# Kernel optimization log

Hardware: AMD Instinct MI355X
Metric: run time of the kernel (lower is better)

The kernel has to match this reference:

```python
import jax, jax.numpy as jnp
import numpy as np

B, T, N, H, L, K, E, KSEL = 16, 24, 2000, 64, 2, 2, 3, 2
OUT_LEN = 24
NUM_MAT = 1 + 2 * K  # identity + K powers of each of the 2 supports


def _rw(adj):
    # random-walk matrix D^{-1} A
    d = adj.sum(axis=1)
    return adj / jnp.where(d == 0, 1.0, d)[:, None]


def _dconv(xh, A_q, A_h, W, b):
    # k-hop dual-direction diffusion convolution; xh: [b,n,f]
    feats = [xh]
    for A in (A_q, A_h):
        cur = xh
        for _ in range(K):
            cur = jnp.einsum('nm,bmf->bnf', A, cur)
            feats.append(cur)
    return jnp.concatenate(feats, axis=-1) @ W + b


def _cell(x, h, A_q, A_h, Wg, bg, Wc, bc):
    # DCRNN (diffusion-conv GRU) cell
    xh = jnp.concatenate([x, h], axis=-1)
    ru = jax.nn.sigmoid(_dconv(xh, A_q, A_h, Wg, bg))
    r, u = jnp.split(ru, 2, axis=-1)
    c = jnp.tanh(_dconv(jnp.concatenate([x, r * h], axis=-1), A_q, A_h, Wc, bc))
    return u * h + (1.0 - u) * c


def setup_inputs() -> dict:
    key = jax.random.key(0)
    ks = jax.random.split(key, 24)
    s = 0.02
    nrm = lambda k, shp: (jax.random.normal(k, shp) * s).astype(jnp.float32)
    adj = (jax.random.uniform(ks[0], (N, N)) * (jax.random.uniform(ks[1], (N, N)) < 0.05)).astype(jnp.float32)
    x_enc = jax.random.normal(ks[2], (B, T, N, 1), dtype=jnp.float32)
    x_enc = x_enc * (jax.random.uniform(ks[3], (B, T, N, 1)) < 0.7)
    x_dec = jax.random.normal(ks[4], (B, OUT_LEN, N, 1), dtype=jnp.float32)

    def cell_p(k, fin):
        k1, k2 = jax.random.split(k)
        fcat = NUM_MAT * (fin + H)
        return (nrm(k1, (fcat, 2 * H)), jnp.zeros(2 * H, jnp.float32),
                nrm(k2, (fcat, H)), jnp.zeros(H, jnp.float32))

    e0 = cell_p(ks[5], 1)
    e1 = cell_p(ks[6], H)
    d0 = cell_p(ks[7], 1)
    d1 = cell_p(ks[8], H)
    return dict(
        adj=adj, x_enc=x_enc, x_dec=x_dec,
        gate_w1=nrm(ks[9], (T, H)), gate_b1=jnp.zeros(H, jnp.float32),
        gate_w2=nrm(ks[10], (H, E)), gate_b2=jnp.zeros(E, jnp.float32),
        ew_mean=nrm(ks[11], (T, T)), eb_mean=jnp.zeros(T, jnp.float32),
        ew_wmean=nrm(ks[12], (T, T)), eb_wmean=jnp.zeros(T, jnp.float32),
        ew_diff=nrm(ks[13], (T, T)), eb_diff=jnp.zeros(T, jnp.float32),
        enc0_Wg=e0[0], enc0_bg=e0[1], enc0_Wc=e0[2], enc0_bc=e0[3],
        enc1_Wg=e1[0], enc1_bg=e1[1], enc1_Wc=e1[2], enc1_bc=e1[3],
        dec0_Wg=d0[0], dec0_bg=d0[1], dec0_Wc=d0[2], dec0_bc=d0[3],
        dec1_Wg=d1[0], dec1_bg=d1[1], dec1_Wc=d1[2], dec1_bc=d1[3],
        fc_w=nrm(ks[14], (H, 1)), fc_b=jnp.zeros(1, jnp.float32),
        epoch=10,
    )


def reference(adj, x_enc, x_dec, gate_w1, gate_b1, gate_w2, gate_b2,
              ew_mean, eb_mean, ew_wmean, eb_wmean, ew_diff, eb_diff,
              enc0_Wg, enc0_bg, enc0_Wc, enc0_bc, enc1_Wg, enc1_bg, enc1_Wc, enc1_bc,
              dec0_Wg, dec0_bg, dec0_Wc, dec0_bc, dec1_Wg, dec1_bg, dec1_Wc, dec1_bc,
              fc_w, fc_b, epoch):
    A_q = _rw(adj)
    A_h = _rw(adj.T)

    # ---- DataPreparation: MoE-gated graph imputation ----
    x = jnp.transpose(x_enc[..., 0], (0, 2, 1))  # [b, n, t]
    g = jax.nn.relu(x @ gate_w1 + gate_b1)
    logits = g @ gate_w2 + gate_b2               # [b, n, E]
    top, idx = jax.lax.top_k(logits, KSEL)
    w = jax.nn.softmax(top, axis=-1)
    gate = (w[..., None] * jax.nn.one_hot(idx, E, dtype=x.dtype)).sum(axis=-2)  # [b,n,E]

    adj_ns = adj * (1.0 - jnp.eye(N, dtype=adj.dtype))
    deg_bin = (adj_ns > 0).astype(x.dtype)
    A_mean = deg_bin / jnp.maximum(deg_bin.sum(axis=1, keepdims=True), 1.0)
    rs = adj_ns.sum(axis=1, keepdims=True)
    A_wmean = adj_ns / jnp.where(rs == 0, 1.0, rs)
    A_diff = _rw(adj_ns)

    outs = [jnp.einsum('nm,bmt->bnt', A_agg, x) @ W + b
            for A_agg, W, b in ((A_mean, ew_mean, eb_mean),
                                (A_wmean, ew_wmean, eb_wmean),
                                (A_diff, ew_diff, eb_diff))]
    combined = (gate[..., None] * jnp.stack(outs, axis=2)).sum(axis=2)  # [b,n,t]
    x = jnp.where(x == 0, combined, x)
    x_imp = jnp.transpose(x, (0, 2, 1))[..., None]  # [b,t,n,1]

    # ---- Encoder: scan over time, 2 DCRNN layers ----
    enc_params = ((enc0_Wg, enc0_bg, enc0_Wc, enc0_bc),
                  (enc1_Wg, enc1_bg, enc1_Wc, enc1_bc))

    def enc_step(h, xt):
        inp = xt
        hs = []
        for l in range(L):
            nh = _cell(inp, h[l], A_q, A_h, *enc_params[l])
            inp = nh
            hs.append(nh)
        return jnp.stack(hs), None

    h0 = jnp.zeros((L, B, N, H), x_imp.dtype)
    hT, _ = jax.lax.scan(enc_step, h0, jnp.transpose(x_imp, (1, 0, 2, 3)))

    dec_params = ((dec0_Wg, dec0_bg, dec0_Wc, dec0_bc),
                  (dec1_Wg, dec1_bg, dec1_Wc, dec1_bc))

    def dec_step(carry, _):
        inp, h = carry
        hs = []
        for l in range(L):
            nh = _cell(inp, h[l], A_q, A_h, *dec_params[l])
            inp = nh
            hs.append(nh)
        out = nh @ fc_w + fc_b  # [b,n,1]
        return (out, jnp.stack(hs)), out

    _, outs_t = jax.lax.scan(dec_step, (x_imp[:, -1], hT), None, length=OUT_LEN)
    return jnp.transpose(outs_t, (1, 0, 2, 3))  # [b, out_len, n, 1]
```

## Files before the change

kernel.cpp:

```cpp
#include <hip/hip_runtime.h>

#define NROW 2000
#define NB   16
#define NT   24
#define NH   64
#define NM   (NROW*NB)
#define HOPLDS (NROW*64)
#define ENT_CAP 262144

typedef _Float16 h16;
typedef __attribute__((ext_vector_type(2))) _Float16 h16x2;
typedef __attribute__((ext_vector_type(8))) _Float16 h16x8;
typedef __attribute__((ext_vector_type(4))) float    f32x4;

__device__ __forceinline__ h16x2 bc_h2(unsigned int u){ union{unsigned int u; h16x2 h;} c; c.u=u; return c.h; }

__global__ __launch_bounds__(256) void k_count(const float* adj, int* cnt_q, int* cnt_h, int* cnt_ns,
    float* rsum_q, float* rsum_h, float* rsum_ns, int* deg_ns){
  int wid = (blockIdx.x*256 + threadIdx.x)>>6;
  int lane = threadIdx.x & 63;
  int kind = wid / NROW, n = wid - kind*NROW;
  int cnt = 0; float sum = 0.f;
  for (int c = lane; c < NROW; c += 64){
    float v = (kind==1) ? adj[(size_t)c*NROW + n] : adj[(size_t)n*NROW + c];
    if (kind==2 && c==n) v = 0.f;
    cnt += (v != 0.f); sum += v;
  }
  for (int off=32; off; off>>=1){ cnt += __shfl_down(cnt,off); sum += __shfl_down(sum,off); }
  if (lane==0){
    int pc = (cnt+7)&~7;
    if (kind==0){ cnt_q[n]=pc; rsum_q[n]=sum; }
    else if (kind==1){ cnt_h[n]=pc; rsum_h[n]=sum; }
    else { cnt_ns[n]=pc; rsum_ns[n]=sum; deg_ns[n]=cnt; }
  }
}

__global__ __launch_bounds__(1024) void k_scan(const int* cq, const int* ch, const int* cn,
    int* rq, int* rh, int* rn){
  __shared__ int s0[2048], s1[2048], s2[2048];
  int t = threadIdx.x;
  for (int a=0;a<2;a++){ int i=t+a*1024; s0[i]= i<NROW?cq[i]:0; s1[i]= i<NROW?ch[i]:0; s2[i]= i<NROW?cn[i]:0; }
  __syncthreads();
  for (int off=1; off<2048; off<<=1){
    int v0[2],v1[2],v2[2];
    for (int a=0;a<2;a++){ int i=t+a*1024; v0[a]= i>=off? s0[i-off]:0; v1[a]= i>=off? s1[i-off]:0; v2[a]= i>=off? s2[i-off]:0; }
    __syncthreads();
    for (int a=0;a<2;a++){ int i=t+a*1024; s0[i]+=v0[a]; s1[i]+=v1[a]; s2[i]+=v2[a]; }
    __syncthreads();
  }
  for (int a=0;a<2;a++){ int i=t+a*1024; if (i<=NROW){ rq[i]= i? s0[i-1]:0; rh[i]= i? s1[i-1]:0; rn[i]= i? s2[i-1]:0; } }
}

__device__ __forceinline__ uint2 mk_ent(int c, float a){
  h16 h = (h16)a;
  unsigned short us = __builtin_bit_cast(unsigned short, h);
  return make_uint2((unsigned int)(c*64), (unsigned int)us * 0x10001u);
}

__global__ __launch_bounds__(256) void k_fill(const float* adj, const int* rptr_q, const int* rptr_h, const int* rptr_ns,
    const float* rsum_q, const float* rsum_h, const float* rsum_ns, const int* deg_ns,
    uint2* ent_q, uint2* ent_h, uint2* ent_m, uint2* ent_w){
  int wid = (blockIdx.x*256 + threadIdx.x)>>6;
  int lane = threadIdx.x & 63;
  int kind = wid / NROW, n = wid - kind*NROW;
  const int* rp = (kind==0)?rptr_q:(kind==1)?rptr_h:rptr_ns;
  int p = rp[n], pend = rp[n+1];
  float inv, invm = 0.f;
  if (kind==0){ float d = rsum_q[n]; inv = d!=0.f?1.f/d:0.f; }
  else if (kind==1){ float d = rsum_h[n]; inv = d!=0.f?1.f/d:0.f; }
  else { float d = rsum_ns[n]; inv = d!=0.f?1.f/d:0.f; int dg = deg_ns[n]; invm = 1.f/(float)(dg>1?dg:1); }
  int base = 0;
  unsigned long long below = (1ull<<lane)-1ull;
  for (int c0=0; c0<NROW; c0+=64){
    int c = c0+lane; float v = 0.f;
    if (c < NROW){ v = (kind==1)? adj[(size_t)c*NROW+n] : adj[(size_t)n*NROW+c]; if (kind==2 && c==n) v = 0.f; }
    unsigned long long m = __ballot(v != 0.f);
    if (v != 0.f){
      int pos = p + base + __popcll(m & below);
      if (kind==2){ ent_w[pos] = mk_ent(c, v*inv); ent_m[pos] = mk_ent(c, invm); }
      else if (kind==0) ent_q[pos] = mk_ent(c, v*inv);
      else              ent_h[pos] = mk_ent(c, v*inv);
    }
    base += __popcll(m);
  }
  for (int i = p+base+lane; i < pend; i += 64){
    uint2 z = make_uint2(0u,0u);
    if (kind==2){ ent_w[i]=z; ent_m[i]=z; } else if (kind==0) ent_q[i]=z; else ent_h[i]=z;
  }
}

struct HopJob { const h16* X; const int* rptr; const uint2* ent; h16* out; };

__device__ __forceinline__ void proc2(const char* xs, int cl, uint4 p, h16x2 ha[4]){
  union{f32x4 v; h16x2 h[4];} ca, cb;
  ca.v = *(const f32x4*)(xs + p.x + cl);
  cb.v = *(const f32x4*)(xs + p.z + cl);
  h16x2 va = bc_h2(p.y), vb = bc_h2(p.w);
  ha[0] = ca.h[0]*va + ha[0];
  ha[1] = ca.h[1]*va + ha[1];
  ha[2] = ca.h[2]*va + ha[2];
  ha[3] = ca.h[3]*va + ha[3];
  ha[0] = cb.h[0]*vb + ha[0];
  ha[1] = cb.h[1]*vb + ha[1];
  ha[2] = cb.h[2]*vb + ha[2];
  ha[3] = cb.h[3]*vb + ha[3];
}

__global__ __launch_bounds__(1024) void k_hop(HopJob j0, HopJob j1, HopJob j2, HopJob j3,
                                              int coltiles, int rsplit, int rows_per, int C){
  extern __shared__ char xs[];
  int per = coltiles*rsplit;
  int bid = blockIdx.x;
  int jb = bid/per, rem = bid - jb*per;
  int ct = rem/rsplit, rs = rem - ct*rsplit;
  HopJob j = (jb==0)?j0:(jb==1)?j1:(jb==2)?j2:j3;
  int c0 = ct*32;
  int tid = threadIdx.x;
  {
    int r0 = tid>>2, so = tid&3;
    const char* src = (const char*)j.X + (size_t)2*(c0 + so*8);
    char* dst = xs + so*16;
    for (int r = r0; r < NROW; r += 256)
      *(f32x4*)(dst + r*64) = *(const f32x4*)(src + (size_t)2*r*C);
  }
  __syncthreads();
  int lane = tid&63, wv = tid>>6;
  int g = lane>>2;
  int cl = (lane&3)*16;
  int rbase = rs*rows_per;
  int rend = rbase + rows_per; if (rend > NROW) rend = NROW;
  int units = (rows_per+15)>>4;
  for (int u = wv; u < units; u += 16){
    int n = rbase + u*16 + g;
    if (n < rend){
      int p0 = j.rptr[n], cnt = j.rptr[n+1]-p0;
      const uint4* ep4 = (const uint4*)(j.ent + p0);
      float f[8] = {0.f,0.f,0.f,0.f,0.f,0.f,0.f,0.f};
      if (cnt > 0){
        uint4 cur[8];
        #pragma unroll
        for (int u2=0;u2<8;u2++) cur[u2] = ep4[u2];
        int i = 0;
        for (; i+16 <= cnt; i += 16){
          uint4 nx[8];
          int b = (i>>1)+8;
          #pragma unroll
          for (int u2=0;u2<8;u2++) nx[u2] = ep4[b+u2];
          h16x2 ha[4] = {{(_Float16)0.f,(_Float16)0.f},{(_Float16)0.f,(_Float16)0.f},
                         {(_Float16)0.f,(_Float16)0.f},{(_Float16)0.f,(_Float16)0.f}};
          #pragma unroll
          for (int u2=0;u2<8;u2++) proc2(xs, cl, cur[u2], ha);
          f[0] += (float)ha[0][0]; f[1] += (float)ha[0][1];
          f[2] += (float)ha[1][0]; f[3] += (float)ha[1][1];
          f[4] += (float)ha[2][0]; f[5] += (float)ha[2][1];
          f[6] += (float)ha[3][0]; f[7] += (float)ha[3][1];
          #pragma unroll
          for (int u2=0;u2<8;u2++) cur[u2] = nx[u2];
        }
        if (i < cnt){
          h16x2 ha[4] = {{(_Float16)0.f,(_Float16)0.f},{(_Float16)0.f,(_Float16)0.f},
                         {(_Float16)0.f,(_Float16)0.f},{(_Float16)0.f,(_Float16)0.f}};
          proc2(xs, cl, cur[0], ha);
          proc2(xs, cl, cur[1], ha);
          proc2(xs, cl, cur[2], ha);
          proc2(xs, cl, cur[3], ha);
          f[0] += (float)ha[0][0]; f[1] += (float)ha[0][1];
          f[2] += (float)ha[1][0]; f[3] += (float)ha[1][1];
          f[4] += (float)ha[2][0]; f[5] += (float)ha[2][1];
          f[6] += (float)ha[3][0]; f[7] += (float)ha[3][1];
        }
      }
      alignas(16) h16 ov[8];
      #pragma unroll
      for (int k2=0;k2<8;k2++) ov[k2] = (h16)f[k2];
      *(uint4*)((char*)j.out + (size_t)2*((size_t)n*C + c0) + cl) = *(const uint4*)ov;
    }
  }
}

__global__ void k_evinit(const float* rq, const float* rh, float* eq, float* eh){
  int n = blockIdx.x*256+threadIdx.x; if (n>=NROW) return;
  eq[n] = rq[n]!=0.f?1.f:0.f; eh[n] = rh[n]!=0.f?1.f:0.f;
}

__global__ __launch_bounds__(256) void k_matvec(const int* rptr, const uint2* ent, const float* vin, float* vout){
  int wid = (blockIdx.x*256+threadIdx.x)>>6; int lane = threadIdx.x&63;
  if (wid >= NROW) return;
  int p0 = rptr[wid], p1 = rptr[wid+1];
  float s = 0.f;
  for (int i=p0+lane; i<p1; i+=64){
    uint2 e = ent[i];
    int idx = (int)(e.x>>6);
    h16 hv = __builtin_bit_cast(h16, (unsigned short)(e.y & 0xffffu));
    s += (float)hv * vin[idx];
  }
  for (int off=32; off; off>>=1) s += __shfl_down(s,off);
  if (lane==0) vout[wid] = s;
}

__global__ void k_bias2(const float* W, const float* fcb, const float* e1, const float* e2,
                        const float* e3, const float* e4, float* dst, int O){
  int idx = blockIdx.x*256+threadIdx.x; if (idx >= NROW*O) return;
  int n = idx/O, o = idx - n*O;
  float v = W[o] + e1[n]*W[(size_t)65*O+o] + e2[n]*W[(size_t)130*O+o]
                 + e3[n]*W[(size_t)195*O+o] + e4[n]*W[(size_t)260*O+o];
  dst[idx] = fcb[0]*v;
}

__global__ void k_wpack(const float* W, const float* fcw, h16* dst, int O, int nch, int mode){
  int idx = blockIdx.x*256+threadIdx.x; if (idx >= nch*O*32) return;
  int k = idx&31; int o = (idx>>5)%O; int ch = idx/(O*32);
  float v = 0.f;
  if (mode==0){
    if (ch < 10){ int m = ch>>1, j = (ch&1)*32 + k; v = W[(size_t)(m*65+1+j)*O + o]; }
    else if (k < 5) v = W[(size_t)(k*65)*O + o];
  } else if (mode==1){
    int m = ch>>2, j = (ch&3)*32 + k; v = W[(size_t)(m*128+j)*O + o];
  } else {
    if (ch < 10){ int m = ch>>1, j = (ch&1)*32 + k; v = fcw[j]*W[(size_t)(m*65)*O + o]; }
    else { int c2 = ch-10; int m = c2>>1, j = (c2&1)*32 + k; v = W[(size_t)(m*65+1+j)*O + o]; }
  }
  dst[(size_t)(ch*O + o)*32 + k] = (h16)v;
}

__global__ __launch_bounds__(256) void k_impute_gate(const float* x_enc, const float* gw1, const float* gb1,
    const float* gw2, const float* gb2, float* gate3, h16* xT){
  int tid = blockIdx.x*256+threadIdx.x; if (tid >= NM) return;
  int b = tid / NROW, n = tid - b*NROW;
  float x24[NT];
  #pragma unroll
  for (int t=0;t<NT;t++) x24[t] = x_enc[((size_t)b*NT+t)*NROW + n];
  float acc[NH];
  #pragma unroll
  for (int h=0;h<NH;h++) acc[h] = gb1[h];
  for (int t=0;t<NT;t++){
    float xv = x24[t];
    #pragma unroll
    for (int h=0;h<NH;h++) acc[h] = fmaf(xv, gw1[t*NH+h], acc[h]);
  }
  #pragma unroll
  for (int h=0;h<NH;h++) acc[h] = fmaxf(acc[h], 0.f);
  float lg[3];
  #pragma unroll
  for (int e=0;e<3;e++){
    float s = gb2[e];
    #pragma unroll
    for (int h=0;h<NH;h++) s = fmaf(acc[h], gw2[h*3+e], s);
    lg[e] = s;
  }
  int i0 = 0; if (lg[1] > lg[0]) i0 = 1; if (lg[2] > lg[i0]) i0 = 2;
  int i1 = (i0==0)?1:0;
  for (int e=0;e<3;e++) if (e!=i0 && e!=i1 && lg[e] > lg[i1]) i1 = e;
  float w1 = expf(lg[i1]-lg[i0]);
  float s = 1.f + w1;
  float g[3] = {0.f,0.f,0.f};
  g[i0] = 1.f/s; g[i1] = w1/s;
  gate3[tid*3+0]=g[0]; gate3[tid*3+1]=g[1]; gate3[tid*3+2]=g[2];
  h16* xp = xT + ((size_t)n*NB + b)*NT;
  #pragma unroll
  for (int t=0;t<NT;t++) xp[t] = (h16)x24[t];
}

__global__ __launch_bounds__(256) void k_impute_combine(const float* x_enc, const h16* Zm, const h16* Zw,
    const float* gate3, const float* ewm, const float* ebm, const float* eww, const float* ebw,
    const float* ewd, const float* ebd, h16* ximp){
  int tid = blockIdx.x*256+threadIdx.x; if (tid >= NM) return;
  int b = tid / NROW, n = tid - b*NROW;
  float x24[NT], zm[NT], zw[NT];
  const h16* zp1 = Zm + ((size_t)n*NB+b)*NT;
  const h16* zp2 = Zw + ((size_t)n*NB+b)*NT;
  #pragma unroll
  for (int t=0;t<NT;t++){ x24[t] = x_enc[((size_t)b*NT+t)*NROW + n]; zm[t]=(float)zp1[t]; zw[t]=(float)zp2[t]; }
  float g0=gate3[tid*3], g1=gate3[tid*3+1], g2=gate3[tid*3+2];
  h16* op = ximp + ((size_t)n*NB+b)*NT;
  for (int t=0;t<NT;t++){
    float am=ebm[t], aw=ebw[t], ad=ebd[t];
    #pragma unroll
    for (int ss=0;ss<NT;ss++){ am = fmaf(zm[ss], ewm[ss*NT+t], am); aw = fmaf(zw[ss], eww[ss*NT+t], aw); ad = fmaf(zw[ss], ewd[ss*NT+t], ad); }
    float comb = g0*am + g1*aw + g2*ad;
    op[t] = (h16)((x24[t]==0.f)? comb : x24[t]);
  }
}

__global__ void k_xpack8(const h16* ximp, const h16* xq1, const h16* xq2, const h16* xh1, const h16* xh2, h16* xp){
  int idx = blockIdx.x*256+threadIdx.x; if (idx >= NT*NM) return;
  int t = idx/NM, r = idx - t*NM;
  size_t s = (size_t)r*NT + t;
  alignas(16) h16 v[8] = { ximp[s], xq1[s], xq2[s], xh1[s], xh2[s], (h16)0.f,(h16)0.f,(h16)0.f };
  *(uint4*)(xp + ((size_t)t*NM + r)*8) = *(const uint4*)v;
}

struct GArgs {
  const h16* src[20];
  int rstrideB[20];
  int coffB[20];
  const h16* wpack;
  const float* bias;
  const h16* hbuf;
  h16* rhbuf;
  float* ubuf;
  h16* hout;
  const float* bias2;
  const float* fcw;
  const float* fcb;
  float* dout;
  int tstep;
  int nchunks;
  int xchunk;
};

template<int O, int GATE, int BIAS2, int FCOUT>
__global__ __launch_bounds__(256) void k_g(GArgs a){
  __shared__ h16 As[64*40];
  __shared__ h16 Bs[O*40];
  const int tid = threadIdx.x;
  const int lane = tid&63, wv = tid>>6;
  const int l15 = lane&15, l4 = lane>>4;
  const int mbase = blockIdx.x*64;
  f32x4 acc[O/16];
  #pragma unroll
  for (int cf=0;cf<O/16;cf++) acc[cf] = (f32x4){0.f,0.f,0.f,0.f};

  f32x4 ra, rb[O/64 > 0 ? O/64 : 1];
  const f32x4 vz = (f32x4){0.f,0.f,0.f,0.f};
  const int r_ = tid>>2, q_ = tid&3;
  auto loadA = [&](int ch){
    const char* sp = (const char*)a.src[ch] + a.coffB[ch] + (size_t)mbase*a.rstrideB[ch];
    if (ch == a.xchunk){
      ra = q_ ? vz : *(const f32x4*)(sp + (size_t)r_*16);
    } else {
      int rs = a.rstrideB[ch];
      ra = *(const f32x4*)(sp + (size_t)r_*rs + q_*16);
    }
    const char* wp = (const char*)a.wpack + (size_t)ch*O*64;
    #pragma unroll
    for (int ps=0; ps<O/64; ps++){
      int flat = ps*256+tid;
      rb[ps] = *(const f32x4*)(wp + (size_t)flat*16);
    }
  };
  auto writeA = [&](int ch){
    *(f32x4*)((char*)As + r_*80 + q_*16) = ra;
    #pragma unroll
    for (int ps=0; ps<O/64; ps++){
      int flat = ps*256+tid; int r = flat>>2, q = flat&3;
      *(f32x4*)((char*)Bs + r*80 + q*16) = rb[ps];
    }
  };

  loadA(0);
  for (int ch=0; ch<a.nchunks; ch++){
    writeA(ch);
    __syncthreads();
    if (ch+1 < a.nchunks) loadA(ch+1);
    h16x8 a0 = *(const h16x8*)((const char*)As + (wv*16 + l15)*80 + l4*16);
    #pragma unroll
    for (int cf=0; cf<O/16; cf++){
      h16x8 bfr = *(const h16x8*)((const char*)Bs + (cf*16 + l15)*80 + l4*16);
      acc[cf] = __builtin_amdgcn_mfma_f32_16x16x32_f16(a0, bfr, acc[cf], 0,0,0);
    }
    __syncthreads();
  }
  float fcp[4] = {0.f,0.f,0.f,0.f};
  #pragma unroll
  for (int cf=0; cf<O/16; cf++){
    #pragma unroll
    for (int i=0;i<4;i++){
      int row = mbase + wv*16 + l4*4 + i;
      int col = cf*16 + l15;
      float v = acc[cf][i] + a.bias[col];
      if (BIAS2) v += a.bias2[(size_t)(row>>4)*O + col];
      if (GATE){
        float sg = 1.f/(1.f+expf(-v));
        if (cf*16 < NH){
          float hv = (float)a.hbuf[(size_t)row*NH + col];
          a.rhbuf[(size_t)row*NH + col] = (h16)(sg*hv);
        } else {
          a.ubuf[(size_t)row*NH + (col-NH)] = sg;
        }
      } else {
        float cc = tanhf(v);
        float u  = a.ubuf[(size_t)row*NH + col];
        float hv = (float)a.hbuf[(size_t)row*NH + col];
        float hn = u*hv + (1.f-u)*cc;
        a.hout[(size_t)row*NH + col] = (h16)hn;
        if (FCOUT) fcp[i] += hn * a.fcw[col];
      }
    }
  }
  if (FCOUT){
    #pragma unroll
    for (int k=0;k<4;k++){
      float s = fcp[k];
      s += __shfl_xor(s,1); s += __shfl_xor(s,2); s += __shfl_xor(s,4); s += __shfl_xor(s,8);
      if (l15==0){
        int row = mbase + wv*16 + l4*4 + k;
        int n = row>>4, b = row&15;
        a.dout[(size_t)b*(NT*NROW) + (size_t)a.tstep*NROW + n] = s + a.fcb[0];
      }
    }
  }
}

extern "C" void kernel_launch(void* const* d_in, const int* in_sizes, int n_in,
                              void* d_out, int out_size, void* d_ws, size_t ws_size,
                              hipStream_t stream)
{
  const float* adj   = (const float*)d_in[0];
  const float* x_enc = (const float*)d_in[1];
  const float* gw1   = (const float*)d_in[3];
  const float* gb1   = (const float*)d_in[4];
  const float* gw2   = (const float*)d_in[5];
  const float* gb2   = (const float*)d_in[6];
  const float* ewm   = (const float*)d_in[7];
  const float* ebm   = (const float*)d_in[8];
  const float* eww   = (const float*)d_in[9];
  const float* ebw   = (const float*)d_in[10];
  const float* ewd   = (const float*)d_in[11];
  const float* ebd   = (const float*)d_in[12];
  const float* Wg[4] = {(const float*)d_in[13],(const float*)d_in[17],(const float*)d_in[21],(const float*)d_in[25]};
  const float* bg[4] = {(const float*)d_in[14],(const float*)d_in[18],(const float*)d_in[22],(const float*)d_in[26]};
  const float* Wc[4] = {(const float*)d_in[15],(const float*)d_in[19],(const float*)d_in[23],(const float*)d_in[27]};
  const float* bc[4] = {(const float*)d_in[16],(const float*)d_in[20],(const float*)d_in[24],(const float*)d_in[28]};
  const float* fcw   = (const float*)d_in[29];
  const float* fcb   = (const float*)d_in[30];
  float* outp = (float*)d_out;
  (void)in_sizes; (void)n_in; (void)out_size; (void)ws_size;

  char* base = (char*)d_ws;
  size_t off = 0;
  auto alloc = [&](size_t sz)->char*{ char* p = base + off; off += (sz + 255) & ~(size_t)255; return p; };

  uint2* ent_q = (uint2*)alloc(ENT_CAP*8);
  uint2* ent_h = (uint2*)alloc(ENT_CAP*8);
  uint2* ent_m = (uint2*)alloc(ENT_CAP*8);
  uint2* ent_w = (uint2*)alloc(ENT_CAP*8);
  int* rptr_q = (int*)alloc(2001*4);
  int* rptr_h = (int*)alloc(2001*4);
  int* rptr_n = (int*)alloc(2001*4);
  int* cnt_q = (int*)alloc(NROW*4);
  int* cnt_h = (int*)alloc(NROW*4);
  int* cnt_n = (int*)alloc(NROW*4);
  float* rsum_q = (float*)alloc(NROW*4);
  float* rsum_h = (float*)alloc(NROW*4);
  float* rsum_n = (float*)alloc(NROW*4);
  int* deg_n = (int*)alloc(NROW*4);
  float* evq1 = (float*)alloc(NROW*4);
  float* evq2 = (float*)alloc(NROW*4);
  float* evh1 = (float*)alloc(NROW*4);
  float* evh2 = (float*)alloc(NROW*4);
  float* gate3 = (float*)alloc((size_t)NM*3*4);
  h16* xpack = (h16*)alloc((size_t)NT*NM*8*2);
  h16* wp_e0g = (h16*)alloc(11*128*64); h16* wp_e0c = (h16*)alloc(11*64*64);
  h16* wp_e1g = (h16*)alloc(20*128*64); h16* wp_e1c = (h16*)alloc(20*64*64);
  h16* wp_d0gE= (h16*)alloc(11*128*64); h16* wp_d0cE= (h16*)alloc(11*64*64);
  h16* wp_d0gW= (h16*)alloc(20*128*64); h16* wp_d0cW= (h16*)alloc(20*64*64);
  h16* wp_d1g = (h16*)alloc(20*128*64); h16* wp_d1c = (h16*)alloc(20*64*64);
  float* bias2g = (float*)alloc((size_t)NROW*128*4);
  float* bias2c = (float*)alloc((size_t)NROW*64*4);
  const size_t SEG = (size_t)NM*NH*2;
  h16* h0 = (h16*)alloc(SEG);
  h16* h1 = (h16*)alloc(SEG);
  float* ub = (float*)alloc((size_t)NM*NH*4);
  h16* rh = (h16*)alloc(SEG);
  h16* zb = (h16*)alloc(SEG);
  h16* H0Q1=(h16*)alloc(SEG); h16* H0Q2=(h16*)alloc(SEG); h16* H0H1=(h16*)alloc(SEG); h16* H0H2=(h16*)alloc(SEG);
  h16* H1Q1=(h16*)alloc(SEG); h16* H1Q2=(h16*)alloc(SEG); h16* H1H1=(h16*)alloc(SEG); h16* H1H2=(h16*)alloc(SEG);
  h16* RHQ1=(h16*)alloc(SEG); h16* RHQ2=(h16*)alloc(SEG); h16* RHH1=(h16*)alloc(SEG); h16* RHH2=(h16*)alloc(SEG);
  h16* xT   = RHQ1;  h16* Zm = RHQ2;  h16* Zw = RHH1;  h16* ximp = RHH2;
  h16* xq1  = H1Q1;  h16* xq2 = H1Q2; h16* xh1 = H1H1; h16* xh2 = H1H2;

  hipFuncSetAttribute(reinterpret_cast<const void*>(k_hop),
                      hipFuncAttributeMaxDynamicSharedMemorySize, HOPLDS);

  hipMemsetAsync(zb, 0, SEG, stream);
  hipMemsetAsync(h0, 0, SEG, stream);
  hipMemsetAsync(h1, 0, SEG, stream);

  k_count<<<1500,256,0,stream>>>(adj, cnt_q, cnt_h, cnt_n, rsum_q, rsum_h, rsum_n, deg_n);
  k_scan<<<1,1024,0,stream>>>(cnt_q, cnt_h, cnt_n, rptr_q, rptr_h, rptr_n);
  k_fill<<<1500,256,0,stream>>>(adj, rptr_q, rptr_h, rptr_n, rsum_q, rsum_h, rsum_n, deg_n,
                                ent_q, ent_h, ent_m, ent_w);
  k_evinit<<<8,256,0,stream>>>(rsum_q, rsum_h, evq1, evh1);
  k_matvec<<<500,256,0,stream>>>(rptr_q, ent_q, evq1, evq2);
  k_matvec<<<500,256,0,stream>>>(rptr_h, ent_h, evh1, evh2);
  k_bias2<<<1000,256,0,stream>>>(Wg[2], fcb, evq1, evq2, evh1, evh2, bias2g, 128);
  k_bias2<<<500,256,0,stream>>>(Wc[2], fcb, evq1, evq2, evh1, evh2, bias2c, 64);
  auto wpk = [&](const float* W, h16* dst, int O, int nch, int mode){
    k_wpack<<<(nch*O*32+255)/256,256,0,stream>>>(W, fcw, dst, O, nch, mode);
  };
  wpk(Wg[0], wp_e0g, 128, 11, 0); wpk(Wc[0], wp_e0c, 64, 11, 0);
  wpk(Wg[1], wp_e1g, 128, 20, 1); wpk(Wc[1], wp_e1c, 64, 20, 1);
  wpk(Wg[2], wp_d0gE,128, 11, 0); wpk(Wc[2], wp_d0cE,64, 11, 0);
  wpk(Wg[2], wp_d0gW,128, 20, 2); wpk(Wc[2], wp_d0cW,64, 20, 2);
  wpk(Wg[3], wp_d1g, 128, 20, 1); wpk(Wc[3], wp_d1c, 64, 20, 1);

  k_impute_gate<<<125,256,0,stream>>>(x_enc, gw1, gb1, gw2, gb2, gate3, xT);

  auto hop = [&](HopJob a, HopJob b, HopJob c, HopJob d, int nj, int C, int rsplit){
    int ct = C/32;
    k_hop<<<nj*ct*rsplit, 1024, HOPLDS, stream>>>(a,b,c,d, ct, rsplit, NROW/rsplit, C);
  };
  HopJob JA{xT, rptr_n, ent_m, Zm}, JB{xT, rptr_n, ent_w, Zw};
  hop(JA, JB, JA, JB, 2, NB*NT, 10);
  k_impute_combine<<<125,256,0,stream>>>(x_enc, Zm, Zw, gate3, ewm, ebm, eww, ebw, ewd, ebd, ximp);
  HopJob X1{ximp, rptr_q, ent_q, xq1}, X2{ximp, rptr_h, ent_h, xh1};
  hop(X1, X2, X1, X2, 2, NB*NT, 10);
  HopJob X3{xq1, rptr_q, ent_q, xq2}, X4{xh1, rptr_h, ent_h, xh2};
  hop(X3, X4, X3, X4, 2, NB*NT, 10);
  k_xpack8<<<(NT*NM+255)/256,256,0,stream>>>(ximp, xq1, xq2, xh1, xh2, xpack);

  h16* HSEG0[5] = {h0, H0Q1, H0Q2, H0H1, H0H2};
  h16* HSEG1[5] = {h1, H1Q1, H1Q2, H1H1, H1H2};
  h16* RSEG[5]  = {rh, RHQ1, RHQ2, RHH1, RHH2};
  h16* ZSEG[5]  = {zb, zb, zb, zb, zb};

  auto shapeA = [&](GArgs& A, h16* const* seg, const h16* xpk){
    for (int m=0;m<5;m++) for (int s=0;s<2;s++){ int ch=2*m+s; A.src[ch]=seg[m]; A.rstrideB[ch]=NH*2; A.coffB[ch]=s*64; }
    A.src[10]=xpk; A.rstrideB[10]=16; A.coffB[10]=0; A.nchunks=11; A.xchunk=10;
  };
  auto shapeB = [&](GArgs& A, h16* const* sa, h16* const* sb){
    for (int m=0;m<5;m++) for (int s=0;s<4;s++){ int ch=4*m+s;
      A.src[ch] = (s<2)? sa[m] : sb[m]; A.rstrideB[ch]=NH*2; A.coffB[ch]=(s&1)*64; }
    A.nchunks=20; A.xchunk=-1;
  };
  auto shapeC = [&](GArgs& A, h16* const* segH, h16* const* segX){
    for (int m=0;m<5;m++) for (int s=0;s<2;s++){
      int ch=2*m+s; A.src[ch]=segX[m]; A.rstrideB[ch]=NH*2; A.coffB[ch]=s*64;
      int c2=10+2*m+s; A.src[c2]=segH[m]; A.rstrideB[c2]=NH*2; A.coffB[c2]=s*64; }
    A.nchunks=20; A.xchunk=-1;
  };
  auto common = [&](GArgs& A, const h16* wp, const float* bias, const h16* hb, const float* b2, int t){
    A.wpack=wp; A.bias=bias; A.hbuf=hb; A.rhbuf=rh; A.ubuf=ub; A.hout=(h16*)hb;
    A.bias2=b2; A.fcw=fcw; A.fcb=fcb; A.dout=outp; A.tstep=t;
  };

  for (int phase=0; phase<2; phase++){
    int ig = phase? 2 : 0;
    const h16* wpg0E = phase? wp_d0gE : wp_e0g;
    const h16* wpc0E = phase? wp_d0cE : wp_e0c;
    const h16* wpg1  = phase? wp_d1g  : wp_e1g;
    const h16* wpc1  = phase? wp_d1c  : wp_e1c;
    for (int t=0;t<NT;t++){
      bool wprime = (phase==1 && t>0);
      if (wprime){
        HopJob a{h1, rptr_q, ent_q, H1Q1}, b{h1, rptr_h, ent_h, H1H1};
        hop(a,b,a,b, 2, NB*NH, 4);
        HopJob c{H1Q1, rptr_q, ent_q, H1Q2}, d{H1H1, rptr_h, ent_h, H1H2};
        hop(c,d,c,d, 2, NB*NH, 4);
      }
      {
        GArgs A{};
        if (wprime) shapeC(A, HSEG0, HSEG1);
        else shapeA(A, (phase==0 && t==0)? ZSEG : HSEG0, xpack + (size_t)((phase==0)? t : 23)*NM*8);
        common(A, wprime? wp_d0gW : wpg0E, bg[ig], h0, bias2g, t);
        if (wprime) k_g<128,1,1,0><<<500,256,0,stream>>>(A);
        else        k_g<128,1,0,0><<<500,256,0,stream>>>(A);
      }
      if (wprime){
        HopJob a{rh, rptr_q, ent_q, RHQ1}, b{rh, rptr_h, ent_h, RHH1};
        hop(a,b,a,b, 2, NB*NH, 4);
        HopJob c{RHQ1, rptr_q, ent_q, RHQ2}, d{RHH1, rptr_h, ent_h, RHH2};
        hop(c,d,c,d, 2, NB*NH, 4);
      } else {
        HopJob a{rh, rptr_q, ent_q, RHQ1}, b{rh, rptr_h, ent_h, RHH1};
        HopJob c{h1, rptr_q, ent_q, H1Q1}, d{h1, rptr_h, ent_h, H1H1};
        hop(a,b,c,d, 4, NB*NH, 2);
        HopJob a2{RHQ1, rptr_q, ent_q, RHQ2}, b2{RHH1, rptr_h, ent_h, RHH2};
        HopJob c2{H1Q1, rptr_q, ent_q, H1Q2}, d2{H1H1, rptr_h, ent_h, H1H2};
        hop(a2,b2,c2,d2, 4, NB*NH, 2);
      }
      {
        GArgs A{};
        if (wprime) shapeC(A, RSEG, HSEG1);
        else shapeA(A, RSEG, xpack + (size_t)((phase==0)? t : 23)*NM*8);
        common(A, wprime? wp_d0cW : wpc0E, bc[ig], h0, bias2c, t);
        if (wprime) k_g<64,0,1,0><<<500,256,0,stream>>>(A);
        else        k_g<64,0,0,0><<<500,256,0,stream>>>(A);
      }
      {
        HopJob a{h0, rptr_q, ent_q, H0Q1}, b{h0, rptr_h, ent_h, H0H1};
        hop(a,b,a,b, 2, NB*NH, 4);
        HopJob c{H0Q1, rptr_q, ent_q, H0Q2}, d{H0H1, rptr_h, ent_h, H0H2};
        hop(c,d,c,d, 2, NB*NH, 4);
      }
      {
        GArgs A{};
        shapeB(A, HSEG0, HSEG1);
        common(A, wpg1, bg[ig+1], h1, nullptr, t);
        k_g<128,1,0,0><<<500,256,0,stream>>>(A);
      }
      {
        HopJob a{rh, rptr_q, ent_q, RHQ1}, b{rh, rptr_h, ent_h, RHH1};
        hop(a,b,a,b, 2, NB*NH, 4);
        HopJob c{RHQ1, rptr_q, ent_q, RHQ2}, d{RHH1, rptr_h, ent_h, RHH2};
        hop(c,d,c,d, 2, NB*NH, 4);
      }
      {
        GArgs A{};
        shapeB(A, HSEG0, RSEG);
        common(A, wpc1, bc[ig+1], h1, nullptr, t);
        if (phase) k_g<64,0,0,1><<<500,256,0,stream>>>(A);
        else       k_g<64,0,0,0><<<500,256,0,stream>>>(A);
      }
    }
  }
}
```

Measured before the change: 13.50 ms.

## Degree-sort rows for SpMM load balance and drop LDS staging in GEMM

Adds a bucket sort of rows by nonzero count, so each 16-row group in the sparse hop kernel processes rows of similar degree. Row groups are interleaved across row splits to even out work. Separately, the gate GEMM kernel now loads MFMA fragments straight from global memory into registers with double buffering, replacing the LDS tiles and barriers. Each wave now computes a 64-row by O/4-column tile, and the FC output is reduced across waves through shared memory. The risks are scattered output row order, which can hurt write locality, and more global load traffic, since fragments are no longer shared through LDS.

Result: slower. 15.51 ms (+14.9%).

```diff
diff --git a/kernel.cpp b/kernel.cpp
--- a/kernel.cpp
+++ b/kernel.cpp
@@ -49,6 +49,29 @@
     __syncthreads();
   }
   for (int a=0;a<2;a++){ int i=t+a*1024; if (i<=NROW){ rq[i]= i? s0[i-1]:0; rh[i]= i? s1[i-1]:0; rn[i]= i? s2[i-1]:0; } }
+}
+
+__global__ __launch_bounds__(1024) void k_sort(const int* c0, const int* c1, const int* c2,
+                                               int* o0, int* o1, int* o2){
+  const int* cnt = blockIdx.x==0 ? c0 : blockIdx.x==1 ? c1 : c2;
+  int* order     = blockIdx.x==0 ? o0 : blockIdx.x==1 ? o1 : o2;
+  __shared__ int hist[256];
+  __shared__ int offs[256];
+  int tid = threadIdx.x;
+  if (tid < 256) hist[tid] = 0;
+  __syncthreads();
+  for (int r = tid; r < NROW; r += 1024){
+    int b = cnt[r] >> 4; if (b > 255) b = 255;
+    atomicAdd(&hist[b], 1);
+  }
+  __syncthreads();
+  if (tid == 0){ int s = 0; for (int i=0;i<256;i++){ offs[i] = s; s += hist[i]; } }
+  __syncthreads();
+  for (int r = tid; r < NROW; r += 1024){
+    int b = cnt[r] >> 4; if (b > 255) b = 255;
+    int p = atomicAdd(&offs[b], 1);
+    order[p] = r;
+  }
 }
 
 __device__ __forceinline__ uint2 mk_ent(int c, float a){
@@ -89,7 +112,7 @@
   }
 }
 
-struct HopJob { const h16* X; const int* rptr; const uint2* ent; h16* out; };
+struct HopJob { const h16* X; const int* rptr; const uint2* ent; const int* order; h16* out; };
 
 __device__ __forceinline__ void proc2(const char* xs, int cl, uint4 p, h16x2 ha[4]){
   union{f32x4 v; h16x2 h[4];} ca, cb;
@@ -107,7 +130,7 @@
 }
 
 __global__ __launch_bounds__(1024) void k_hop(HopJob j0, HopJob j1, HopJob j2, HopJob j3,
-                                              int coltiles, int rsplit, int rows_per, int C){
+                                              int coltiles, int rsplit, int C){
   extern __shared__ char xs[];
   int per = coltiles*rsplit;
   int bid = blockIdx.x;
@@ -127,12 +150,11 @@
   int lane = tid&63, wv = tid>>6;
   int g = lane>>2;
   int cl = (lane&3)*16;
-  int rbase = rs*rows_per;
-  int rend = rbase + rows_per; if (rend > NROW) rend = NROW;
-  int units = (rows_per+15)>>4;
-  for (int u = wv; u < units; u += 16){
-    int n = rbase + u*16 + g;
-    if (n < rend){
+  for (int k = wv; ; k += 16){
+    int gu = rs + k*rsplit;
+    if (gu >= 125) break;
+    int n = j.order[gu*16 + g];
+    {
       int p0 = j.rptr[n], cnt = j.rptr[n+1]-p0;
       const uint4* ep4 = (const uint4*)(j.ent + p0);
       float f[8] = {0.f,0.f,0.f,0.f,0.f,0.f,0.f,0.f};
@@ -311,93 +333,109 @@
 
 template<int O, int GATE, int BIAS2, int FCOUT>
 __global__ __launch_bounds__(256) void k_g(GArgs a){
-  __shared__ h16 As[64*40];
-  __shared__ h16 Bs[O*40];
+  __shared__ float fcred[64*4];
   const int tid = threadIdx.x;
   const int lane = tid&63, wv = tid>>6;
   const int l15 = lane&15, l4 = lane>>4;
   const int mbase = blockIdx.x*64;
-  f32x4 acc[O/16];
-  #pragma unroll
-  for (int cf=0;cf<O/16;cf++) acc[cf] = (f32x4){0.f,0.f,0.f,0.f};
-
-  f32x4 ra, rb[O/64 > 0 ? O/64 : 1];
-  const f32x4 vz = (f32x4){0.f,0.f,0.f,0.f};
-  const int r_ = tid>>2, q_ = tid&3;
-  auto loadA = [&](int ch){
-    const char* sp = (const char*)a.src[ch] + a.coffB[ch] + (size_t)mbase*a.rstrideB[ch];
+  const int cbase = wv*(O/4);
+  constexpr int NCF = O/64;
+  f32x4 acc[4][NCF];
+  #pragma unroll
+  for (int rf=0;rf<4;rf++)
+    #pragma unroll
+    for (int cf=0;cf<NCF;cf++) acc[rf][cf] = (f32x4){0.f,0.f,0.f,0.f};
+
+  h16x8 afA[4], bfA[NCF], afB[4], bfB[NCF];
+  const h16x8 hz = {(_Float16)0.f,(_Float16)0.f,(_Float16)0.f,(_Float16)0.f,
+                    (_Float16)0.f,(_Float16)0.f,(_Float16)0.f,(_Float16)0.f};
+
+  auto loadCh = [&](int ch, h16x8 (&af)[4], h16x8 (&bf)[NCF]){
+    const char* sp = (const char*)a.src[ch] + a.coffB[ch];
     if (ch == a.xchunk){
-      ra = q_ ? vz : *(const f32x4*)(sp + (size_t)r_*16);
+      #pragma unroll
+      for (int rf=0; rf<4; rf++){
+        int row = mbase + rf*16 + l15;
+        af[rf] = (l4==0) ? *(const h16x8*)(sp + (size_t)row*16) : hz;
+      }
     } else {
       int rs = a.rstrideB[ch];
-      ra = *(const f32x4*)(sp + (size_t)r_*rs + q_*16);
+      #pragma unroll
+      for (int rf=0; rf<4; rf++){
+        int row = mbase + rf*16 + l15;
+        af[rf] = *(const h16x8*)(sp + (size_t)row*rs + l4*16);
+      }
     }
     const char* wp = (const char*)a.wpack + (size_t)ch*O*64;
     #pragma unroll
-    for (int ps=0; ps<O/64; ps++){
-      int flat = ps*256+tid;
-      rb[ps] = *(const f32x4*)(wp + (size_t)flat*16);
+    for (int cf=0; cf<NCF; cf++)
+      bf[cf] = *(const h16x8*)(wp + (size_t)(cbase + cf*16 + l15)*64 + l4*16);
+  };
+  auto domfma = [&](h16x8 (&af)[4], h16x8 (&bf)[NCF]){
+    #pragma unroll
+    for (int rf=0; rf<4; rf++)
+      #pragma unroll
+      for (int cf=0; cf<NCF; cf++)
+        acc[rf][cf] = __builtin_amdgcn_mfma_f32_16x16x32_f16(af[rf], bf[cf], acc[rf][cf], 0,0,0);
+  };
+
+  loadCh(0, afA, bfA);
+  for (int ch=0; ch<a.nchunks; ch+=2){
+    if (ch+1 < a.nchunks) loadCh(ch+1, afB, bfB);
+    domfma(afA, bfA);
+    if (ch+2 < a.nchunks) loadCh(ch+2, afA, bfA);
+    if (ch+1 < a.nchunks) domfma(afB, bfB);
+  }
+
+  float fcp[16];
+  #pragma unroll
+  for (int k=0;k<16;k++) fcp[k]=0.f;
+  #pragma unroll
+  for (int rf=0; rf<4; rf++){
+    #pragma unroll
+    for (int cf=0; cf<NCF; cf++){
+      #pragma unroll
+      for (int i=0;i<4;i++){
+        int row = mbase + rf*16 + l4*4 + i;
+        int col = cbase + cf*16 + l15;
+        float v = acc[rf][cf][i] + a.bias[col];
+        if (BIAS2) v += a.bias2[(size_t)(row>>4)*O + col];
+        if (GATE){
+          float sg = 1.f/(1.f+expf(-v));
+          if (cbase + cf*16 < NH){
+            float hv = (float)a.hbuf[(size_t)row*NH + col];
+            a.rhbuf[(size_t)row*NH + col] = (h16)(sg*hv);
+          } else {
+            a.ubuf[(size_t)row*NH + (col-NH)] = sg;
+          }
+        } else {
+          float cc = tanhf(v);
+          float u  = a.ubuf[(size_t)row*NH + col];
+          float hv = (float)a.hbuf[(size_t)row*NH + col];
+          float hn = u*hv + (1.f-u)*cc;
+          a.hout[(size_t)row*NH + col] = (h16)hn;
+          if (FCOUT) fcp[rf*4+i] += hn * a.fcw[col];
+        }
+      }
     }
-  };
-  auto writeA = [&](int ch){
-    *(f32x4*)((char*)As + r_*80 + q_*16) = ra;
-    #pragma unroll
-    for (int ps=0; ps<O/64; ps++){
-      int flat = ps*256+tid; int r = flat>>2, q = flat&3;
-      *(f32x4*)((char*)Bs + r*80 + q*16) = rb[ps];
-    }
-  };
-
-  loadA(0);
-  for (int ch=0; ch<a.nchunks; ch++){
-    writeA(ch);
-    __syncthreads();
-    if (ch+1 < a.nchunks) loadA(ch+1);
-    h16x8 a0 = *(const h16x8*)((const char*)As + (wv*16 + l15)*80 + l4*16);
-    #pragma unroll
-    for (int cf=0; cf<O/16; cf++){
-      h16x8 bfr = *(const h16x8*)((const char*)Bs + (cf*16 + l15)*80 + l4*16);
-      acc[cf] = __builtin_amdgcn_mfma_f32_16x16x32_f16(a0, bfr, acc[cf], 0,0,0);
-    }
-    __syncthreads();
-  }
-  float fcp[4] = {0.f,0.f,0.f,0.f};
-  #pragma unroll
-  for (int cf=0; cf<O/16; cf++){
-    #pragma unroll
-    for (int i=0;i<4;i++){
-      int row = mbase + wv*16 + l4*4 + i;
-      int col = cf*16 + l15;
-      float v = acc[cf][i] + a.bias[col];
-      if (BIAS2) v += a.bias2[(size_t)(row>>4)*O + col];
-      if (GATE){
-        float sg = 1.f/(1.f+expf(-v));
-        if (cf*16 < NH){
-          float hv = (float)a.hbuf[(size_t)row*NH + col];
-          a.rhbuf[(size_t)row*NH + col] = (h16)(sg*hv);
-        } else {
-          a.ubuf[(size_t)row*NH + (col-NH)] = sg;
-        }
-      } else {
-        float cc = tanhf(v);
-        float u  = a.ubuf[(size_t)row*NH + col];
-        float hv = (float)a.hbuf[(size_t)row*NH + col];
-        float hn = u*hv + (1.f-u)*cc;
-        a.hout[(size_t)row*NH + col] = (h16)hn;
-        if (FCOUT) fcp[i] += hn * a.fcw[col];
-      }
-    }
   }
   if (FCOUT){
     #pragma unroll
-    for (int k=0;k<4;k++){
+    for (int k=0;k<16;k++){
       float s = fcp[k];
       s += __shfl_xor(s,1); s += __shfl_xor(s,2); s += __shfl_xor(s,4); s += __shfl_xor(s,8);
       if (l15==0){
-        int row = mbase + wv*16 + l4*4 + k;
-        int n = row>>4, b = row&15;
-        a.dout[(size_t)b*(NT*NROW) + (size_t)a.tstep*NROW + n] = s + a.fcb[0];
-      }
+        int rf = k>>2, i = k&3;
+        int row = rf*16 + l4*4 + i;
+        fcred[row*4 + wv] = s;
+      }
+    }
+    __syncthreads();
+    if (tid < 64){
+      float s = fcred[tid*4] + fcred[tid*4+1] + fcred[tid*4+2] + fcred[tid*4+3];
+      int row = mbase + tid;
+      int n = row>>4, b = row&15;
+      a.dout[(size_t)b*(NT*NROW) + (size_t)a.tstep*NROW + n] = s + a.fcb[0];
     }
   }
 }
@@ -441,6 +479,9 @@
   int* cnt_q = (int*)alloc(NROW*4);
   int* cnt_h = (int*)alloc(NROW*4);
   int* cnt_n = (int*)alloc(NROW*4);
+  int* ord_q = (int*)alloc(NROW*4);
+  int* ord_h = (int*)alloc(NROW*4);
+  int* ord_n = (int*)alloc(NROW*4);
   float* rsum_q = (float*)alloc(NROW*4);
   float* rsum_h = (float*)alloc(NROW*4);
   float* rsum_n = (float*)alloc(NROW*4);
@@ -478,6 +519,7 @@
   hipMemsetAsync(h1, 0, SEG, stream);
 
   k_count<<<1500,256,0,stream>>>(adj, cnt_q, cnt_h, cnt_n, rsum_q, rsum_h, rsum_n, deg_n);
+  k_sort<<<3,1024,0,stream>>>(cnt_q, cnt_h, cnt_n, ord_q, ord_h, ord_n);
   k_scan<<<1,1024,0,stream>>>(cnt_q, cnt_h, cnt_n, rptr_q, rptr_h, rptr_n);
   k_fill<<<1500,256,0,stream>>>(adj, rptr_q, rptr_h, rptr_n, rsum_q, rsum_h, rsum_n, deg_n,
                                 ent_q, ent_h, ent_m, ent_w);
@@ -499,14 +541,14 @@
 
   auto hop = [&](HopJob a, HopJob b, HopJob c, HopJob d, int nj, int C, int rsplit){
     int ct = C/32;
-    k_hop<<<nj*ct*rsplit, 1024, HOPLDS, stream>>>(a,b,c,d, ct, rsplit, NROW/rsplit, C);
-  };
-  HopJob JA{xT, rptr_n, ent_m, Zm}, JB{xT, rptr_n, ent_w, Zw};
+    k_hop<<<nj*ct*rsplit, 1024, HOPLDS, stream>>>(a,b,c,d, ct, rsplit, C);
+  };
+  HopJob JA{xT, rptr_n, ent_m, ord_n, Zm}, JB{xT, rptr_n, ent_w, ord_n, Zw};
   hop(JA, JB, JA, JB, 2, NB*NT, 10);
   k_impute_combine<<<125,256,0,stream>>>(x_enc, Zm, Zw, gate3, ewm, ebm, eww, ebw, ewd, ebd, ximp);
-  HopJob X1{ximp, rptr_q, ent_q, xq1}, X2{ximp, rptr_h, ent_h, xh1};
+  HopJob X1{ximp, rptr_q, ent_q, ord_q, xq1}, X2{ximp, rptr_h, ent_h, ord_h, xh1};
   hop(X1, X2, X1, X2, 2, NB*NT, 10);
-  HopJob X3{xq1, rptr_q, ent_q, xq2}, X4{xh1, rptr_h, ent_h, xh2};
+  HopJob X3{xq1, rptr_q, ent_q, ord_q, xq2}, X4{xh1, rptr_h, ent_h, ord_h, xh2};
   hop(X3, X4, X3, X4, 2, NB*NT, 10);
   k_xpack8<<<(NT*NM+255)/256,256,0,stream>>>(ximp, xq1, xq2, xh1, xh2, xpack);
 
@@ -544,9 +586,9 @@
     for (int t=0;t<NT;t++){
       bool wprime = (phase==1 && t>0);
       if (wprime){
-        HopJob a{h1, rptr_q, ent_q, H1Q1}, b{h1, rptr_h, ent_h, H1H1};
+        HopJob a{h1, rptr_q, ent_q, ord_q, H1Q1}, b{h1, rptr_h, ent_h, ord_h, H1H1};
         hop(a,b,a,b, 2, NB*NH, 4);
-        HopJob c{H1Q1, rptr_q, ent_q, H1Q2}, d{H1H1, rptr_h, ent_h, H1H2};
+        HopJob c{H1Q1, rptr_q, ent_q, ord_q, H1Q2}, d{H1H1, rptr_h, ent_h, ord_h, H1H2};
         hop(c,d,c,d, 2, NB*NH, 4);
       }
       {
@@ -558,16 +600,16 @@
         else        k_g<128,1,0,0><<<500,256,0,stream>>>(A);
       }
       if (wprime){
-        HopJob a{rh, rptr_q, ent_q, RHQ1}, b{rh, rptr_h, ent_h, RHH1};
+        HopJob a{rh, rptr_q, ent_q, ord_q, RHQ1}, b{rh, rptr_h, ent_h, ord_h, RHH1};
         hop(a,b,a,b, 2, NB*NH, 4);
-        HopJob c{RHQ1, rptr_q, ent_q, RHQ2}, d{RHH1, rptr_h, ent_h, RHH2};
+        HopJob c{RHQ1, rptr_q, ent_q, ord_q, RHQ2}, d{RHH1, rptr_h, ent_h, ord_h, RHH2};
         hop(c,d,c,d, 2, NB*NH, 4);
       } else {
-        HopJob a{rh, rptr_q, ent_q, RHQ1}, b{rh, rptr_h, ent_h, RHH1};
-        HopJob c{h1, rptr_q, ent_q, H1Q1}, d{h1, rptr_h, ent_h, H1H1};
+        HopJob a{rh, rptr_q, ent_q, ord_q, RHQ1}, b{rh, rptr_h, ent_h, ord_h, RHH1};
+        HopJob c{h1, rptr_q, ent_q, ord_q, H1Q1}, d{h1, rptr_h, ent_h, ord_h, H1H1};
         hop(a,b,c,d, 4, NB*NH, 2);
-        HopJob a2{RHQ1, rptr_q, ent_q, RHQ2}, b2{RHH1, rptr_h, ent_h, RHH2};
-        HopJob c2{H1Q1, rptr_q, ent_q, H1Q2}, d2{H1H1, rptr_h, ent_h, H1H2};
+        HopJob a2{RHQ1, rptr_q, ent_q, ord_q, RHQ2}, b2{RHH1, rptr_h, ent_h, ord_h, RHH2};
+        HopJob c2{H1Q1, rptr_q, ent_q, ord_q, H1Q2}, d2{H1H1, rptr_h, ent_h, ord_h, H1H2};
         hop(a2,b2,c2,d2, 4, NB*NH, 2);
       }
       {
@@ -579,9 +621,9 @@
         else        k_g<64,0,0,0><<<500,256,0,stream>>>(A);
       }
       {
-        HopJob a{h0, rptr_q, ent_q, H0Q1}, b{h0, rptr_h, ent_h, H0H1};
+        HopJob a{h0, rptr_q, ent_q, ord_q, H0Q1}, b{h0, rptr_h, ent_h, ord_h, H0H1};
         hop(a,b,a,b, 2, NB*NH, 4);
-        HopJob c{H0Q1, rptr_q, ent_q, H0Q2}, d{H0H1, rptr_h, ent_h, H0H2};
+        HopJob c{H0Q1, rptr_q, ent_q, ord_q, H0Q2}, d{H0H1, rptr_h, ent_h, ord_h, H0H2};
         hop(c,d,c,d, 2, NB*NH, 4);
       }
       {
@@ -591,9 +633,9 @@
         k_g<128,1,0,0><<<500,256,0,stream>>>(A);
       }
       {
-        HopJob a{rh, rptr_q, ent_q, RHQ1}, b{rh, rptr_h, ent_h, RHH1};
+        HopJob a{rh, rptr_q, ent_q, ord_q, RHQ1}, b{rh, rptr_h, ent_h, ord_h, RHH1};
         hop(a,b,a,b, 2, NB*NH, 4);
-        HopJob c{RHQ1, rptr_q, ent_q, RHQ2}, d{RHH1, rptr_h, ent_h, RHH2};
+        HopJob c{RHQ1, rptr_q, ent_q, ord_q, RHQ2}, d{RHH1, rptr_h, ent_h, ord_h, RHH2};
         hop(c,d,c,d, 2, NB*NH, 4);
       }
       {
```

## Bucket-sort rows by nonzero count and interleave row groups across hop blocks

Applied to the files above, without the earlier changes.

Adds a one-time k_sort kernel that bucket-sorts adjacency rows by their nonzero count (in buckets of 16). The SpMM hop kernel then takes its rows through this order and assigns 16-row units to blocks round-robin instead of as contiguous ranges. Rows with similar degree now share a wave, which should cut lane divergence within a wave and even out work across blocks. The cost is one extra indirection load per row and less locality in output writes.

New measurement: 13.03 ms. 3.4% less time.

```diff
diff --git a/kernel.cpp b/kernel.cpp
--- a/kernel.cpp
+++ b/kernel.cpp
@@ -49,6 +49,29 @@
     __syncthreads();
   }
   for (int a=0;a<2;a++){ int i=t+a*1024; if (i<=NROW){ rq[i]= i? s0[i-1]:0; rh[i]= i? s1[i-1]:0; rn[i]= i? s2[i-1]:0; } }
+}
+
+__global__ __launch_bounds__(1024) void k_sort(const int* c0, const int* c1, const int* c2,
+                                               int* o0, int* o1, int* o2){
+  const int* cnt = blockIdx.x==0 ? c0 : blockIdx.x==1 ? c1 : c2;
+  int* order     = blockIdx.x==0 ? o0 : blockIdx.x==1 ? o1 : o2;
+  __shared__ int hist[256];
+  __shared__ int offs[256];
+  int tid = threadIdx.x;
+  if (tid < 256) hist[tid] = 0;
+  __syncthreads();
+  for (int r = tid; r < NROW; r += 1024){
+    int b = cnt[r] >> 4; if (b > 255) b = 255;
+    atomicAdd(&hist[b], 1);
+  }
+  __syncthreads();
+  if (tid == 0){ int s = 0; for (int i=0;i<256;i++){ offs[i] = s; s += hist[i]; } }
+  __syncthreads();
+  for (int r = tid; r < NROW; r += 1024){
+    int b = cnt[r] >> 4; if (b > 255) b = 255;
+    int p = atomicAdd(&offs[b], 1);
+    order[p] = r;
+  }
 }
 
 __device__ __forceinline__ uint2 mk_ent(int c, float a){
@@ -89,7 +112,7 @@
   }
 }
 
-struct HopJob { const h16* X; const int* rptr; const uint2* ent; h16* out; };
+struct HopJob { const h16* X; const int* rptr; const uint2* ent; const int* order; h16* out; };
 
 __device__ __forceinline__ void proc2(const char* xs, int cl, uint4 p, h16x2 ha[4]){
   union{f32x4 v; h16x2 h[4];} ca, cb;
@@ -107,7 +130,7 @@
 }
 
 __global__ __launch_bounds__(1024) void k_hop(HopJob j0, HopJob j1, HopJob j2, HopJob j3,
-                                              int coltiles, int rsplit, int rows_per, int C){
+                                              int coltiles, int rsplit, int C){
   extern __shared__ char xs[];
   int per = coltiles*rsplit;
   int bid = blockIdx.x;
@@ -127,12 +150,11 @@
   int lane = tid&63, wv = tid>>6;
   int g = lane>>2;
   int cl = (lane&3)*16;
-  int rbase = rs*rows_per;
-  int rend = rbase + rows_per; if (rend > NROW) rend = NROW;
-  int units = (rows_per+15)>>4;
-  for (int u = wv; u < units; u += 16){
-    int n = rbase + u*16 + g;
-    if (n < rend){
+  for (int k = wv; ; k += 16){
+    int gu = rs + k*rsplit;
+    if (gu >= 125) break;
+    int n = j.order[gu*16 + g];
+    {
       int p0 = j.rptr[n], cnt = j.rptr[n+1]-p0;
       const uint4* ep4 = (const uint4*)(j.ent + p0);
       float f[8] = {0.f,0.f,0.f,0.f,0.f,0.f,0.f,0.f};
@@ -441,6 +463,9 @@
   int* cnt_q = (int*)alloc(NROW*4);
   int* cnt_h = (int*)alloc(NROW*4);
   int* cnt_n = (int*)alloc(NROW*4);
+  int* ord_q = (int*)alloc(NROW*4);
+  int* ord_h = (int*)alloc(NROW*4);
+  int* ord_n = (int*)alloc(NROW*4);
   float* rsum_q = (float*)alloc(NROW*4);
   float* rsum_h = (float*)alloc(NROW*4);
   float* rsum_n = (float*)alloc(NROW*4);
@@ -478,6 +503,7 @@
   hipMemsetAsync(h1, 0, SEG, stream);
 
   k_count<<<1500,256,0,stream>>>(adj, cnt_q, cnt_h, cnt_n, rsum_q, rsum_h, rsum_n, deg_n);
+  k_sort<<<3,1024,0,stream>>>(cnt_q, cnt_h, cnt_n, ord_q, ord_h, ord_n);
   k_scan<<<1,1024,0,stream>>>(cnt_q, cnt_h, cnt_n, rptr_q, rptr_h, rptr_n);
   k_fill<<<1500,256,0,stream>>>(adj, rptr_q, rptr_h, rptr_n, rsum_q, rsum_h, rsum_n, deg_n,
                                 ent_q, ent_h, ent_m, ent_w);
@@ -499,14 +525,14 @@
 
   auto hop = [&](HopJob a, HopJob b, HopJob c, HopJob d, int nj, int C, int rsplit){
     int ct = C/32;
-    k_hop<<<nj*ct*rsplit, 1024, HOPLDS, stream>>>(a,b,c,d, ct, rsplit, NROW/rsplit, C);
-  };
-  HopJob JA{xT, rptr_n, ent_m, Zm}, JB{xT, rptr_n, ent_w, Zw};
+    k_hop<<<nj*ct*rsplit, 1024, HOPLDS, stream>>>(a,b,c,d, ct, rsplit, C);
+  };
+  HopJob JA{xT, rptr_n, ent_m, ord_n, Zm}, JB{xT, rptr_n, ent_w, ord_n, Zw};
   hop(JA, JB, JA, JB, 2, NB*NT, 10);
   k_impute_combine<<<125,256,0,stream>>>(x_enc, Zm, Zw, gate3, ewm, ebm, eww, ebw, ewd, ebd, ximp);
-  HopJob X1{ximp, rptr_q, ent_q, xq1}, X2{ximp, rptr_h, ent_h, xh1};
+  HopJob X1{ximp, rptr_q, ent_q, ord_q, xq1}, X2{ximp, rptr_h, ent_h, ord_h, xh1};
   hop(X1, X2, X1, X2, 2, NB*NT, 10);
-  HopJob X3{xq1, rptr_q, ent_q, xq2}, X4{xh1, rptr_h, ent_h, xh2};
+  HopJob X3{xq1, rptr_q, ent_q, ord_q, xq2}, X4{xh1, rptr_h, ent_h, ord_h, xh2};
   hop(X3, X4, X3, X4, 2, NB*NT, 10);
   k_xpack8<<<(NT*NM+255)/256,256,0,stream>>>(ximp, xq1, xq2, xh1, xh2, xpack);
 
@@ -544,9 +570,9 @@
     for (int t=0;t<NT;t++){
       bool wprime = (phase==1 && t>0);
       if (wprime){
-        HopJob a{h1, rptr_q, ent_q, H1Q1}, b{h1, rptr_h, ent_h, H1H1};
+        HopJob a{h1, rptr_q, ent_q, ord_q, H1Q1}, b{h1, rptr_h, ent_h, ord_h, H1H1};
         hop(a,b,a,b, 2, NB*NH, 4);
-        HopJob c{H1Q1, rptr_q, ent_q, H1Q2}, d{H1H1, rptr_h, ent_h, H1H2};
+        HopJob c{H1Q1, rptr_q, ent_q, ord_q, H1Q2}, d{H1H1, rptr_h, ent_h, ord_h, H1H2};
         hop(c,d,c,d, 2, NB*NH, 4);
       }
       {
@@ -558,16 +584,16 @@
         else        k_g<128,1,0,0><<<500,256,0,stream>>>(A);
       }
       if (wprime){
-        HopJob a{rh, rptr_q, ent_q, RHQ1}, b{rh, rptr_h, ent_h, RHH1};
+        HopJob a{rh, rptr_q, ent_q, ord_q, RHQ1}, b{rh, rptr_h, ent_h, ord_h, RHH1};
         hop(a,b,a,b, 2, NB*NH, 4);
-        HopJob c{RHQ1, rptr_q, ent_q, RHQ2}, d{RHH1, rptr_h, ent_h, RHH2};
+        HopJob c{RHQ1, rptr_q, ent_q, ord_q, RHQ2}, d{RHH1, rptr_h, ent_h, ord_h, RHH2};
         hop(c,d,c,d, 2, NB*NH, 4);
       } else {
-        HopJob a{rh, rptr_q, ent_q, RHQ1}, b{rh, rptr_h, ent_h, RHH1};
-        HopJob c{h1, rptr_q, ent_q, H1Q1}, d{h1, rptr_h, ent_h, H1H1};
+        HopJob a{rh, rptr_q, ent_q, ord_q, RHQ1}, b{rh, rptr_h, ent_h, ord_h, RHH1};
+        HopJob c{h1, rptr_q, ent_q, ord_q, H1Q1}, d{h1, rptr_h, ent_h, ord_h, H1H1};
         hop(a,b,c,d, 4, NB*NH, 2);
-        HopJob a2{RHQ1, rptr_q, ent_q, RHQ2}, b2{RHH1, rptr_h, ent_h, RHH2};
-        HopJob c2{H1Q1, rptr_q, ent_q, H1Q2}, d2{H1H1, rptr_h, ent_h, H1H2};
+        HopJob a2{RHQ1, rptr_q, ent_q, ord_q, RHQ2}, b2{RHH1, rptr_h, ent_h, ord_h, RHH2};
+        HopJob c2{H1Q1, rptr_q, ent_q, ord_q, H1Q2}, d2{H1H1, rptr_h, ent_h, ord_h, H1H2};
         hop(a2,b2,c2,d2, 4, NB*NH, 2);
       }
       {
@@ -579,9 +605,9 @@
         else        k_g<64,0,0,0><<<500,256,0,stream>>>(A);
       }
       {
-        HopJob a{h0, rptr_q, ent_q, H0Q1}, b{h0, rptr_h, ent_h, H0H1};
+        HopJob a{h0, rptr_q, ent_q, ord_q, H0Q1}, b{h0, rptr_h, ent_h, ord_h, H0H1};
         hop(a,b,a,b, 2, NB*NH, 4);
-        HopJob c{H0Q1, rptr_q, ent_q, H0Q2}, d{H0H1, rptr_h, ent_h, H0H2};
+        HopJob c{H0Q1, rptr_q, ent_q, ord_q, H0Q2}, d{H0H1, rptr_h, ent_h, ord_h, H0H2};
         hop(c,d,c,d, 2, NB*NH, 4);
       }
       {
@@ -591,9 +617,9 @@
         k_g<128,1,0,0><<<500,256,0,stream>>>(A);
       }
       {
-        HopJob a{rh, rptr_q, ent_q, RHQ1}, b{rh, rptr_h, ent_h, RHH1};
+        HopJob a{rh, rptr_q, ent_q, ord_q, RHQ1}, b{rh, rptr_h, ent_h, ord_h, RHH1};
         hop(a,b,a,b, 2, NB*NH, 4);
-        HopJob c{RHQ1, rptr_q, ent_q, RHQ2}, d{RHH1, rptr_h, ent_h, RHH2};
+        HopJob c{RHQ1, rptr_q, ent_q, ord_q, RHQ2}, d{RHH1, rptr_h, ent_h, ord_h, RHH2};
         hop(c,d,c,d, 2, NB*NH, 4);
       }
       {
```
